# Kernel tuning notes

Hardware: AMD Instinct MI355X
Metric: run time of the kernel (lower is better)

The kernel has to match this reference:

```python
import jax, jax.numpy as jnp
import numpy as np


def _blended_linear(h, W, b, blend):
    # Equivalent to building w[b] = sum_e blend[e,b]*W[e] (shape B,out,in)
    # and computing w[b] @ h[b] + sum_e blend[e,b]*b[e], without the huge
    # per-sample weight tensor.
    # h: (B, in), W: (E, out, in), b: (E, out), blend: (E, B) -> (B, out)
    y = jnp.einsum('eoi,bi->ebo', W, h)          # per-expert outputs
    y = jnp.einsum('eb,ebo->bo', blend, y)       # blend across experts
    return y + blend.T @ b                       # blended bias


def setup_inputs() -> dict:
    key = jax.random.key(0)
    ks = jax.random.split(key, 9)
    E, B = 8, 8192
    dims = [480, 512, 512, 363]
    inp = {
        'x': jax.random.normal(ks[0], (B, dims[0]), jnp.float32),
        'weight_blend': jax.random.uniform(ks[1], (E, B), jnp.float32),
        'W1': jax.random.normal(ks[2], (E, dims[1], dims[0]), jnp.float32) * 0.05,
        'b1': jax.random.normal(ks[3], (E, dims[1]), jnp.float32) * 0.05,
        'W2': jax.random.normal(ks[4], (E, dims[2], dims[1]), jnp.float32) * 0.05,
        'b2': jax.random.normal(ks[5], (E, dims[2]), jnp.float32) * 0.05,
        'W3': jax.random.normal(ks[6], (E, dims[3], dims[2]), jnp.float32) * 0.05,
        'b3': jax.random.normal(ks[7], (E, dims[3]), jnp.float32) * 0.05,
        'batch_size': B,
    }
    return inp


def reference(x, weight_blend, W1, b1, W2, b2, W3, b3, batch_size):
    # Dropout layers are identity in eval mode; final_ac=True -> softmax.
    h = _blended_linear(x, W1, b1, weight_blend)
    h = jax.nn.elu(h)
    h = _blended_linear(h, W2, b2, weight_blend)
    h = jax.nn.elu(h)
    h = _blended_linear(h, W3, b3, weight_blend)
    return jax.nn.softmax(h, axis=-1)
```

## Files before the change

### kernel.cpp

```cpp
#include <hip/hip_runtime.h>
#include <cstdint>

#define E_EXP 8
#define BATCH 8192
#define D0 480
#define D1 512
#define D2 512
#define D3 363
#define KP 512
#define N3PAD 384

typedef _Float16 f16x8 __attribute__((ext_vector_type(8)));
typedef float f32x16 __attribute__((ext_vector_type(16)));
typedef unsigned short u16;

#define VMCNT(n) asm volatile("s_waitcnt vmcnt(" #n ")" ::: "memory")

__device__ __forceinline__ u16 f2h(float f) {
    _Float16 h = (_Float16)f;
    return __builtin_bit_cast(u16, h);
}

__device__ __forceinline__ void async16(const u16* g, u16* s) {
    __builtin_amdgcn_global_load_lds(
        reinterpret_cast<const __attribute__((address_space(1))) void*>(
            reinterpret_cast<uintptr_t>(g)),
        reinterpret_cast<__attribute__((address_space(3))) void*>(
            reinterpret_cast<uintptr_t>(s)),
        16, 0, 0);
}

__device__ __forceinline__ void pack_seg(const float* __restrict__ src,
                                         u16* __restrict__ dst,
                                         int OUT_src, int OUTP, int IN_src) {
    int total = E_EXP * OUTP * 128;
    int in4 = IN_src >> 2;
    for (int idx = blockIdx.x * blockDim.x + threadIdx.x; idx < total;
         idx += gridDim.x * blockDim.x) {
        int e = idx / (OUTP * 128);
        int r = idx - e * OUTP * 128;
        int o = r >> 7;
        int k4 = r & 127;
        ushort4 w;
        if (o < OUT_src && k4 < in4) {
            const float4 v = *reinterpret_cast<const float4*>(
                src + ((size_t)e * OUT_src + o) * IN_src + (k4 << 2));
            w.x = f2h(v.x); w.y = f2h(v.y); w.z = f2h(v.z); w.w = f2h(v.w);
        } else {
            w.x = 0; w.y = 0; w.z = 0; w.w = 0;
        }
        *reinterpret_cast<ushort4*>(dst + ((size_t)e * OUTP + o) * KP + (k4 << 2)) = w;
    }
}

__global__ void pack_all(const float* __restrict__ W1, const float* __restrict__ W2,
                         const float* __restrict__ W3, u16* __restrict__ wf1,
                         u16* __restrict__ wf2, u16* __restrict__ wf3) {
    pack_seg(W1, wf1, 512, 512, D0);
    pack_seg(W2, wf2, 512, 512, D1);
    pack_seg(W3, wf3, D3, N3PAD, D2);
}

__global__ void pad_x(const float* __restrict__ x, u16* __restrict__ xp) {
    int total = BATCH * 128;
    for (int idx = blockIdx.x * blockDim.x + threadIdx.x; idx < total;
         idx += gridDim.x * blockDim.x) {
        int b = idx >> 7, k4 = idx & 127;
        ushort4 w;
        if (k4 < 120) {
            const float4 v = *reinterpret_cast<const float4*>(
                x + (size_t)b * D0 + (k4 << 2));
            w.x = f2h(v.x); w.y = f2h(v.y); w.z = f2h(v.z); w.w = f2h(v.w);
        } else {
            w.x = 0; w.y = 0; w.z = 0; w.w = 0;
        }
        *reinterpret_cast<ushort4*>(xp + (size_t)b * KP + (k4 << 2)) = w;
    }
}

__global__ __launch_bounds__(512, 2) void gemm_all(
    const u16* __restrict__ A, const u16* __restrict__ Bw,
    const float* __restrict__ blend, const float* __restrict__ bias,
    u16* __restrict__ out, int OUTP, int OUTR, int nbn, int mode) {
    __shared__ __align__(16) u16 S[73728];
    const int tid = threadIdx.x;
    const int w = tid >> 6, lane = tid & 63;
    const int wm2 = w & 3, wn2 = w >> 2;
    const int l31 = lane & 31, q2 = lane >> 5;

    const int id = blockIdx.x;
    const int xcd = id & 7;
    const int j = id >> 3;
    const int bm = ((j & 3) << 3) + xcd;
    const int bn = j >> 2;

    f32x16 acc[2][2];
#pragma unroll
    for (int mg = 0; mg < 2; ++mg)
#pragma unroll
        for (int kk = 0; kk < 2; ++kk)
#pragma unroll
            for (int i = 0; i < 16; ++i) acc[mg][kk][i] = 0.f;

    _Float16 blh[8][2];
#pragma unroll
    for (int e = 0; e < 8; ++e)
#pragma unroll
        for (int mg = 0; mg < 2; ++mg)
            blh[e][mg] = (_Float16)blend[e * BATCH + bm * 256 + wm2 * 64 +
                                         mg * 32 + l31];

    const int l4r = lane >> 2;
    const int l4s = lane & 3;
    const int ks8 = (l4s ^ ((l4r >> 1) & 3)) << 3;
    const size_t EST = (size_t)OUTP * KP;
    const u16* gA0 = A + (size_t)(bm * 256 + w * 32 + l4r) * KP + ks8;
    const u16* gB0 = Bw + (size_t)w * EST + (size_t)(bn * 64 + l4r) * KP + ks8;
    const size_t R16 = (size_t)16 * KP;
    const int aBase = w * 1024;
    const int bBase = 8192 + w * 2048;

    int aoff[2][2], boff[2];
#pragma unroll
    for (int mg = 0; mg < 2; ++mg) {
        int r = wm2 * 64 + mg * 32 + l31;
        int base = (r >> 4) * 512 + (r & 15) * 32;
        int swz = (r >> 1) & 3;
#pragma unroll
        for (int kk = 0; kk < 2; ++kk)
            aoff[mg][kk] = base + (((kk * 2 + q2) ^ swz) << 3);
    }
    {
        int r = wn2 * 32 + l31;
        int base = (r >> 4) * 512 + (r & 15) * 32;
        int swz = (r >> 1) & 3;
#pragma unroll
        for (int kk = 0; kk < 2; ++kk)
            boff[kk] = base + (((kk * 2 + q2) ^ swz) << 3);
    }

    auto stage = [&](int kt, int b) {
        const int ko = kt << 5;
        u16* buf = S + b * 24576;
        async16(gA0 + ko, buf + aBase);
        async16(gA0 + R16 + ko, buf + aBase + 512);
        async16(gB0 + ko, buf + bBase);
        async16(gB0 + R16 + ko, buf + bBase + 512);
        async16(gB0 + 2 * R16 + ko, buf + bBase + 1024);
        async16(gB0 + 3 * R16 + ko, buf + bBase + 1536);
    };

    stage(0, 0);
    stage(1, 1);
    VMCNT(6);
    __builtin_amdgcn_s_barrier();
    __builtin_amdgcn_sched_barrier(0);

#pragma unroll
    for (int kt = 0; kt < 16; ++kt) {
        const int p = kt % 3;
        if (kt < 14) stage(kt + 2, (kt + 2) % 3);
        const u16* As_ = S + p * 24576;
        const u16* Bs_ = As_ + 8192;
        f16x8 af[2][2];
#pragma unroll
        for (int mg = 0; mg < 2; ++mg)
#pragma unroll
            for (int kk = 0; kk < 2; ++kk)
                af[mg][kk] = *reinterpret_cast<const f16x8*>(&As_[aoff[mg][kk]]);
        __builtin_amdgcn_s_setprio(1);
#pragma unroll
        for (int e = 0; e < 8; ++e) {
            f16x8 bf0 = *reinterpret_cast<const f16x8*>(&Bs_[e * 2048 + boff[0]]);
            f16x8 bf1 = *reinterpret_cast<const f16x8*>(&Bs_[e * 2048 + boff[1]]);
#pragma unroll
            for (int mg = 0; mg < 2; ++mg) {
                f16x8 a0 = af[mg][0] * blh[e][mg];
                acc[mg][0] = __builtin_amdgcn_mfma_f32_32x32x16_f16(
                    a0, bf0, acc[mg][0], 0, 0, 0);
                f16x8 a1 = af[mg][1] * blh[e][mg];
                acc[mg][1] = __builtin_amdgcn_mfma_f32_32x32x16_f16(
                    a1, bf1, acc[mg][1], 0, 0, 0);
            }
        }
        __builtin_amdgcn_s_setprio(0);
        __builtin_amdgcn_sched_barrier(0);
        if (kt < 14) { VMCNT(6); } else { VMCNT(0); }
        __builtin_amdgcn_s_barrier();
        __builtin_amdgcn_sched_barrier(0);
    }

    float* Blf = reinterpret_cast<float*>(S);
    float* Bif = reinterpret_cast<float*>(S + 8192);
    for (int idx = tid; idx < 2048; idx += 512) {
        int e = idx >> 8, r = idx & 255;
        Blf[r * 9 + e] = blend[e * BATCH + bm * 256 + r];
    }
    {
        int e = tid >> 6, c = tid & 63;
        int cg = bn * 64 + c;
        Bif[c * 9 + e] = (cg < OUTR) ? bias[e * OUTR + cg] : 0.f;
    }
    __syncthreads();

    const int col_l = wn2 * 32 + l31;
    const int gcol = bn * 64 + col_l;
    float bif[8];
#pragma unroll
    for (int e = 0; e < 8; ++e) bif[e] = Bif[col_l * 9 + e];
#pragma unroll
    for (int mg = 0; mg < 2; ++mg) {
#pragma unroll
        for (int reg = 0; reg < 16; ++reg) {
            int rloc = (reg & 3) + ((reg >> 2) << 3) + (q2 << 2);
            int rl = wm2 * 64 + mg * 32 + rloc;
            float bb = 0.f;
#pragma unroll
            for (int e = 0; e < 8; ++e) bb += Blf[rl * 9 + e] * bif[e];
            float v = acc[mg][0][reg] + acc[mg][1][reg] + bb;
            if (mode == 0) v = v > 0.f ? v : expm1f(v);
            out[(size_t)(bm * 256 + rl) * OUTP + gcol] = f2h(v);
        }
    }
}

__global__ __launch_bounds__(128) void softmax_rows(
    const u16* __restrict__ P, float* __restrict__ out) {
    const int b = blockIdx.x;
    const int tid = threadIdx.x, lane = tid & 63, w = tid >> 6;
    float v[3];
    int n = 0;
    float mx = -3.4e38f;
    for (int i = tid; i < D3; i += 128) {
        float s = (float)*reinterpret_cast<const _Float16*>(
            P + (size_t)b * N3PAD + i);
        v[n] = s; mx = fmaxf(mx, s); ++n;
    }
#pragma unroll
    for (int off = 32; off >= 1; off >>= 1) mx = fmaxf(mx, __shfl_xor(mx, off, 64));
    __shared__ float sm[4];
    if (lane == 0) sm[w] = mx;
    __syncthreads();
    mx = fmaxf(sm[0], sm[1]);
    float s = 0.f;
    for (int jj = 0; jj < n; ++jj) { v[jj] = expf(v[jj] - mx); s += v[jj]; }
#pragma unroll
    for (int off = 32; off >= 1; off >>= 1) s += __shfl_xor(s, off, 64);
    if (lane == 0) sm[2 + w] = s;
    __syncthreads();
    float inv = 1.f / (sm[2] + sm[3]);
    n = 0;
    for (int i = tid; i < D3; i += 128) { out[(size_t)b * D3 + i] = v[n] * inv; ++n; }
}

extern "C" void kernel_launch(void* const* d_in, const int* in_sizes, int n_in,
                              void* d_out, int out_size, void* d_ws, size_t ws_size,
                              hipStream_t stream) {
    const float* x = (const float*)d_in[0];
    const float* blend = (const float*)d_in[1];
    const float* W1 = (const float*)d_in[2];
    const float* b1 = (const float*)d_in[3];
    const float* W2 = (const float*)d_in[4];
    const float* b2 = (const float*)d_in[5];
    const float* W3 = (const float*)d_in[6];
    const float* b3 = (const float*)d_in[7];
    float* outp = (float*)d_out;

    char* ws = (char*)d_ws;
    u16* wf1 = (u16*)ws; ws += (size_t)E_EXP * 512 * KP * 2;
    u16* wf2 = (u16*)ws; ws += (size_t)E_EXP * 512 * KP * 2;
    u16* wf3 = (u16*)ws; ws += (size_t)E_EXP * N3PAD * KP * 2;
    u16* xp = (u16*)ws;  ws += (size_t)BATCH * KP * 2;
    u16* h1 = (u16*)ws;  ws += (size_t)BATCH * KP * 2;
    u16* h2 = (u16*)ws;  ws += (size_t)BATCH * KP * 2;
    u16* P = (u16*)ws;

    pack_all<<<1024, 256, 0, stream>>>(W1, W2, W3, wf1, wf2, wf3);
    pad_x<<<2048, 256, 0, stream>>>(x, xp);

    gemm_all<<<32 * 8, 512, 0, stream>>>(xp, wf1, blend, b1, h1, 512, 512, 8, 0);
    gemm_all<<<32 * 8, 512, 0, stream>>>(h1, wf2, blend, b2, h2, 512, 512, 8, 0);
    gemm_all<<<32 * 6, 512, 0, stream>>>(h2, wf3, blend, b3, P, N3PAD, D3, 6, 1);
    softmax_rows<<<BATCH, 128, 0, stream>>>(P, outp);
}
```

Before: 222.2 us.

## Split K-tile into four phases interleaving global-to-LDS loads with MFMA clusters

Each K-tile iteration becomes four phases of two experts each. Every phase loads its B fragments from LDS, and the async global-to-LDS copies for tile kt+2 are spread across the first two phases instead of being issued up front. Each phase is bracketed by barriers, with the memory wait moved to the last phase. The goal is a finer-grained, ping-pong-style interleave of memory and MFMA work across waves, at the cost of eight workgroup barriers per K-tile instead of one.

```diff
diff --git a/kernel.cpp b/kernel.cpp
--- a/kernel.cpp
+++ b/kernel.cpp
@@ -159,35 +159,65 @@
 #pragma unroll
     for (int kt = 0; kt < 16; ++kt) {
         const int p = kt % 3;
-        if (kt < 14) stage(kt + 2, (kt + 2) % 3);
         const u16* As_ = S + p * 24576;
         const u16* Bs_ = As_ + 8192;
+        u16* nbuf = S + ((kt + 2) % 3) * 24576;
+        const int ko2 = (kt + 2) << 5;
         f16x8 af[2][2];
 #pragma unroll
-        for (int mg = 0; mg < 2; ++mg)
-#pragma unroll
-            for (int kk = 0; kk < 2; ++kk)
-                af[mg][kk] = *reinterpret_cast<const f16x8*>(&As_[aoff[mg][kk]]);
-        __builtin_amdgcn_s_setprio(1);
-#pragma unroll
-        for (int e = 0; e < 8; ++e) {
-            f16x8 bf0 = *reinterpret_cast<const f16x8*>(&Bs_[e * 2048 + boff[0]]);
-            f16x8 bf1 = *reinterpret_cast<const f16x8*>(&Bs_[e * 2048 + boff[1]]);
-#pragma unroll
-            for (int mg = 0; mg < 2; ++mg) {
-                f16x8 a0 = af[mg][0] * blh[e][mg];
-                acc[mg][0] = __builtin_amdgcn_mfma_f32_32x32x16_f16(
-                    a0, bf0, acc[mg][0], 0, 0, 0);
-                f16x8 a1 = af[mg][1] * blh[e][mg];
-                acc[mg][1] = __builtin_amdgcn_mfma_f32_32x32x16_f16(
-                    a1, bf1, acc[mg][1], 0, 0, 0);
+        for (int ph = 0; ph < 4; ++ph) {
+            if (ph == 0) {
+#pragma unroll
+                for (int mg = 0; mg < 2; ++mg)
+#pragma unroll
+                    for (int kk = 0; kk < 2; ++kk)
+                        af[mg][kk] =
+                            *reinterpret_cast<const f16x8*>(&As_[aoff[mg][kk]]);
             }
+            f16x8 bf[2][2];
+#pragma unroll
+            for (int ee = 0; ee < 2; ++ee)
+#pragma unroll
+                for (int kk = 0; kk < 2; ++kk)
+                    bf[ee][kk] = *reinterpret_cast<const f16x8*>(
+                        &Bs_[(2 * ph + ee) * 2048 + boff[kk]]);
+            if (kt < 14) {
+                if (ph == 0) {
+                    async16(gA0 + ko2, nbuf + aBase);
+                    async16(gA0 + R16 + ko2, nbuf + aBase + 512);
+                    async16(gB0 + ko2, nbuf + bBase);
+                } else if (ph == 1) {
+                    async16(gB0 + R16 + ko2, nbuf + bBase + 512);
+                    async16(gB0 + 2 * R16 + ko2, nbuf + bBase + 1024);
+                    async16(gB0 + 3 * R16 + ko2, nbuf + bBase + 1536);
+                }
+            }
+            __builtin_amdgcn_sched_barrier(0);
+            __builtin_amdgcn_s_barrier();
+            __builtin_amdgcn_sched_barrier(0);
+            __builtin_amdgcn_s_setprio(1);
+#pragma unroll
+            for (int ee = 0; ee < 2; ++ee) {
+                const int e = 2 * ph + ee;
+#pragma unroll
+                for (int mg = 0; mg < 2; ++mg) {
+                    f16x8 a0 = af[mg][0] * blh[e][mg];
+                    acc[mg][0] = __builtin_amdgcn_mfma_f32_32x32x16_f16(
+                        a0, bf[ee][0], acc[mg][0], 0, 0, 0);
+                    f16x8 a1 = af[mg][1] * blh[e][mg];
+                    acc[mg][1] = __builtin_amdgcn_mfma_f32_32x32x16_f16(
+                        a1, bf[ee][1], acc[mg][1], 0, 0, 0);
+                }
+            }
+            __builtin_amdgcn_s_setprio(0);
+            __builtin_amdgcn_sched_barrier(0);
+            if (ph == 3) {
+                if (kt < 14) { VMCNT(6); }
+                else if (kt == 14) { VMCNT(0); }
+            }
+            __builtin_amdgcn_s_barrier();
+            __builtin_amdgcn_sched_barrier(0);
         }
-        __builtin_amdgcn_s_setprio(0);
-        __builtin_amdgcn_sched_barrier(0);
-        if (kt < 14) { VMCNT(6); } else { VMCNT(0); }
-        __builtin_amdgcn_s_barrier();
-        __builtin_amdgcn_sched_barrier(0);
     }
 
     float* Blf = reinterpret_cast<float*>(S);
```

Measured after the change: 226.3 us. Within noise of the previous version (+1.8%).
